# Kernel tuning notes

Measured on AMD Instinct MI355X. Metric: run time of the kernel, lower is better.

Reference implementation:

```python
import jax, jax.numpy as jnp
import numpy as np

KAPPA = 0.5


def setup_inputs() -> dict:
    key = jax.random.key(0)
    embeddings = jax.random.normal(key, (8, 4096, 64), dtype=jnp.float32)
    return {"embeddings": embeddings}


def reference(embeddings):
    # logits[b, n, m] = kappa * <emb[b,n], emb[b,m]>   -> [B, N, N]
    logits = KAPPA * jnp.einsum("bnd,bmd->bnm", embeddings, embeddings)
    B = logits.shape[0]
    # logsumexp over both matrix dims, per batch element
    loss = jax.scipy.special.logsumexp(logits.reshape(B, -1), axis=1)
    return loss.mean()
```

## Files before the change

kernel.cpp:

```cpp
#include <hip/hip_runtime.h>
#include <math.h>

#define BATCH 8
#define NTOK  4096
#define DIM   64
#define BM    128
#define NT    (NTOK / BM)
#define TPB   (NT * (NT + 1) / 2)
#define TOTAL (BATCH * TPB)
#define KAPPA 0.5f
#define LOG2E 1.4426950408889634f
#define LN2   0.6931471805599453f
#define M2FIX 48.0f

typedef _Float16 f16x8 __attribute__((ext_vector_type(8)));
typedef float    f32x16 __attribute__((ext_vector_type(16)));

__device__ __forceinline__ float EXP2(float x) {
#if __has_builtin(__builtin_amdgcn_exp2f)
    return __builtin_amdgcn_exp2f(x);
#else
    return __expf(x * LN2);
#endif
}

__global__ __launch_bounds__(256)
void conv_f16(const float* __restrict__ emb, f16x8* __restrict__ o16) {
    const size_t i = (size_t)blockIdx.x * 256 + threadIdx.x;
    const float4 v0 = *(const float4*)(emb + i * 8);
    const float4 v1 = *(const float4*)(emb + i * 8 + 4);
    f16x8 p;
    p[0] = (_Float16)v0.x; p[1] = (_Float16)v0.y;
    p[2] = (_Float16)v0.z; p[3] = (_Float16)v0.w;
    p[4] = (_Float16)v1.x; p[5] = (_Float16)v1.y;
    p[6] = (_Float16)v1.z; p[7] = (_Float16)v1.w;
    o16[i] = p;
}

__global__ __launch_bounds__(256, 4)
void gram_lse_partial(const f16x8* __restrict__ w16, float* __restrict__ ws) {
    __shared__ f16x8 S[2048];

    const int tid  = threadIdx.x;
    const int lane = tid & 63;
    const int w    = tid >> 6;
    const int p    = blockIdx.x;
    const int bb   = (p & 7) * TPB + (p >> 3);
    const int b    = bb / TPB;
    int t = bb - b * TPB;
    int ti = 0;
    while (t >= NT - ti) { t -= NT - ti; ++ti; }
    const int tj = ti + t;

    const char* pA16 = (const char*)(w16 + ((size_t)b * NTOK + (size_t)ti * BM) * 8);
    const char* pB16 = (const char*)(w16 + ((size_t)b * NTOK + (size_t)tj * BM) * 8);

    {
        const char* pbase  = (w < 2) ? pA16 : pB16;
        const int   upBase = (w & 1) * 512 + lane;
#pragma unroll
        for (int q = 0; q < 8; ++q) {
            const int up  = upBase + q * 64;
            const int g   = up >> 7;
            const int rp  = up & 127;
            const int off = (((rp ^ g) << 7) | (g << 4));
            __builtin_amdgcn_global_load_lds(
                (const __attribute__((address_space(1))) void*)(pbase + off),
                (__attribute__((address_space(3))) void*)&S[(size_t)w * 512 + q * 64],
                16, 0, 0);
        }
    }
    __syncthreads();

    const int half = lane >> 5;
    const int ln31 = lane & 31;
    const int waveR = (w & 1) * 64;
    const int waveC = (w >> 1) * 64;
    const float c2 = KAPPA * LOG2E;

    f32x16 acc00 = {}, acc01 = {}, acc10 = {}, acc11 = {};
#pragma unroll
    for (int s = 0; s < 4; ++s) {
        const int g = 2 * s + half;
        const f16x8 a0 = S[g * BM + ((waveR + ln31) ^ g)];
        const f16x8 a1 = S[g * BM + ((waveR + 32 + ln31) ^ g)];
        const f16x8 b0 = S[1024 + g * BM + ((waveC + ln31) ^ g)];
        const f16x8 b1 = S[1024 + g * BM + ((waveC + 32 + ln31) ^ g)];
        acc00 = __builtin_amdgcn_mfma_f32_32x32x16_f16(a0, b0, acc00, 0, 0, 0);
        acc01 = __builtin_amdgcn_mfma_f32_32x32x16_f16(a0, b1, acc01, 0, 0, 0);
        acc10 = __builtin_amdgcn_mfma_f32_32x32x16_f16(a1, b0, acc10, 0, 0, 0);
        acc11 = __builtin_amdgcn_mfma_f32_32x32x16_f16(a1, b1, acc11, 0, 0, 0);
    }

    float s0 = 0.f, s1 = 0.f, s2 = 0.f, s3 = 0.f;
#pragma unroll
    for (int e = 0; e < 16; ++e) {
        s0 += EXP2(fmaf(c2, acc00[e], -M2FIX));
        s1 += EXP2(fmaf(c2, acc01[e], -M2FIX));
        s2 += EXP2(fmaf(c2, acc10[e], -M2FIX));
        s3 += EXP2(fmaf(c2, acc11[e], -M2FIX));
    }
    float lsum = (s0 + s1) + (s2 + s3);
#pragma unroll
    for (int off = 32; off > 0; off >>= 1)
        lsum += __shfl_xor(lsum, off);

    if (lane == 0) {
        const float wgt = (ti == tj) ? 1.f : 2.f;
        ws[4 * (size_t)bb + w] = wgt * lsum;
    }
}

__global__ __launch_bounds__(512)
void reduce_lse(const float* __restrict__ ws, float* __restrict__ out) {
    const int tid  = threadIdx.x;
    const int w    = tid >> 6;
    const int lane = tid & 63;
    __shared__ float lse8[BATCH];

    const float* p = ws + (size_t)w * TPB * 4;
    float s = 0.f;
#pragma unroll
    for (int c = 0; c < 33; ++c) s += p[lane + 64 * c];
#pragma unroll
    for (int off = 32; off > 0; off >>= 1) s += __shfl_xor(s, off);

    if (lane == 0) lse8[w] = LN2 * (M2FIX + log2f(s));
    __syncthreads();
    if (tid == 0) {
        float a = 0.f;
        for (int i = 0; i < BATCH; ++i) a += lse8[i];
        out[0] = a * (1.f / BATCH);
    }
}

extern "C" void kernel_launch(void* const* d_in, const int* in_sizes, int n_in,
                              void* d_out, int out_size, void* d_ws, size_t ws_size,
                              hipStream_t stream) {
    const float* emb = (const float*)d_in[0];
    float* out = (float*)d_out;
    f16x8* w16 = (f16x8*)d_ws;
    float* prt = (float*)((char*)d_ws + (4u << 20));

    conv_f16<<<NTOK * BATCH * DIM / 8 / 256, 256, 0, stream>>>(emb, w16);
    gram_lse_partial<<<TOTAL, 256, 0, stream>>>(w16, prt);
    reduce_lse<<<1, 512, 0, stream>>>(prt, out);
}
```

Measured before the change: 81.11 us.

## Enlarge Gram tiles to 256x256 with 512-thread blocks

Doubles the tile edge of the symmetric Gram/logsumexp kernel from 128 to 256 rows. Blocks grow to 8 waves, and each wave now computes a 64x128 sub-tile with eight MFMA accumulators. The partial-sum layout and the final reduction are resized to match. The aim is to halve operand-staging traffic per logit and cut block count and launch overhead. In exchange, diagonal tiles waste a slightly larger share of work, each block needs 64KB of LDS, and register pressure is higher.

```diff
diff --git a/kernel.cpp b/kernel.cpp
--- a/kernel.cpp
+++ b/kernel.cpp
@@ -4,10 +4,10 @@
 #define BATCH 8
 #define NTOK  4096
 #define DIM   64
-#define BM    128
-#define NT    (NTOK / BM)
-#define TPB   (NT * (NT + 1) / 2)
-#define TOTAL (BATCH * TPB)
+#define BM    256
+#define NT2   (NTOK / BM)
+#define TPB2  (NT2 * (NT2 + 1) / 2)
+#define TOTAL2 (BATCH * TPB2)
 #define KAPPA 0.5f
 #define LOG2E 1.4426950408889634f
 #define LN2   0.6931471805599453f
@@ -37,32 +37,32 @@
     o16[i] = p;
 }
 
-__global__ __launch_bounds__(256, 4)
+__global__ __launch_bounds__(512, 2)
 void gram_lse_partial(const f16x8* __restrict__ w16, float* __restrict__ ws) {
-    __shared__ f16x8 S[2048];
+    __shared__ f16x8 S[4096];
 
     const int tid  = threadIdx.x;
     const int lane = tid & 63;
     const int w    = tid >> 6;
     const int p    = blockIdx.x;
-    const int bb   = (p & 7) * TPB + (p >> 3);
-    const int b    = bb / TPB;
-    int t = bb - b * TPB;
+    const int b    = p & 7;
+    int t = p >> 3;
     int ti = 0;
-    while (t >= NT - ti) { t -= NT - ti; ++ti; }
+    while (t >= NT2 - ti) { t -= NT2 - ti; ++ti; }
     const int tj = ti + t;
+    const int bbL = b * TPB2 + (p >> 3);
 
     const char* pA16 = (const char*)(w16 + ((size_t)b * NTOK + (size_t)ti * BM) * 8);
     const char* pB16 = (const char*)(w16 + ((size_t)b * NTOK + (size_t)tj * BM) * 8);
 
     {
-        const char* pbase  = (w < 2) ? pA16 : pB16;
-        const int   upBase = (w & 1) * 512 + lane;
+        const char* pbase  = (w < 4) ? pA16 : pB16;
+        const int   upBase = (w & 3) * 512 + lane;
 #pragma unroll
         for (int q = 0; q < 8; ++q) {
             const int up  = upBase + q * 64;
-            const int g   = up >> 7;
-            const int rp  = up & 127;
+            const int g   = up >> 8;
+            const int rp  = up & 255;
             const int off = (((rp ^ g) << 7) | (g << 4));
             __builtin_amdgcn_global_load_lds(
                 (const __attribute__((address_space(1))) void*)(pbase + off),
@@ -74,40 +74,55 @@
 
     const int half = lane >> 5;
     const int ln31 = lane & 31;
-    const int waveR = (w & 1) * 64;
-    const int waveC = (w >> 1) * 64;
+    const int wr   = w >> 1;
+    const int wc   = w & 1;
+    const int rA0  = 64 * wr + ln31, rA1 = rA0 + 32;
+    const int rB0  = 128 * wc + ln31;
     const float c2 = KAPPA * LOG2E;
 
-    f32x16 acc00 = {}, acc01 = {}, acc10 = {}, acc11 = {};
+    f32x16 acc00 = {}, acc01 = {}, acc02 = {}, acc03 = {};
+    f32x16 acc10 = {}, acc11 = {}, acc12 = {}, acc13 = {};
 #pragma unroll
     for (int s = 0; s < 4; ++s) {
         const int g = 2 * s + half;
-        const f16x8 a0 = S[g * BM + ((waveR + ln31) ^ g)];
-        const f16x8 a1 = S[g * BM + ((waveR + 32 + ln31) ^ g)];
-        const f16x8 b0 = S[1024 + g * BM + ((waveC + ln31) ^ g)];
-        const f16x8 b1 = S[1024 + g * BM + ((waveC + 32 + ln31) ^ g)];
+        const int gb = g * 256;
+        const f16x8 a0 = S[gb + (rA0 ^ g)];
+        const f16x8 a1 = S[gb + (rA1 ^ g)];
+        const f16x8 b0 = S[2048 + gb + ((rB0      ) ^ g)];
+        const f16x8 b1 = S[2048 + gb + ((rB0 + 32 ) ^ g)];
+        const f16x8 b2 = S[2048 + gb + ((rB0 + 64 ) ^ g)];
+        const f16x8 b3 = S[2048 + gb + ((rB0 + 96 ) ^ g)];
         acc00 = __builtin_amdgcn_mfma_f32_32x32x16_f16(a0, b0, acc00, 0, 0, 0);
         acc01 = __builtin_amdgcn_mfma_f32_32x32x16_f16(a0, b1, acc01, 0, 0, 0);
+        acc02 = __builtin_amdgcn_mfma_f32_32x32x16_f16(a0, b2, acc02, 0, 0, 0);
+        acc03 = __builtin_amdgcn_mfma_f32_32x32x16_f16(a0, b3, acc03, 0, 0, 0);
         acc10 = __builtin_amdgcn_mfma_f32_32x32x16_f16(a1, b0, acc10, 0, 0, 0);
         acc11 = __builtin_amdgcn_mfma_f32_32x32x16_f16(a1, b1, acc11, 0, 0, 0);
+        acc12 = __builtin_amdgcn_mfma_f32_32x32x16_f16(a1, b2, acc12, 0, 0, 0);
+        acc13 = __builtin_amdgcn_mfma_f32_32x32x16_f16(a1, b3, acc13, 0, 0, 0);
     }
 
     float s0 = 0.f, s1 = 0.f, s2 = 0.f, s3 = 0.f;
+    float s4 = 0.f, s5 = 0.f, s6 = 0.f, s7 = 0.f;
 #pragma unroll
     for (int e = 0; e < 16; ++e) {
         s0 += EXP2(fmaf(c2, acc00[e], -M2FIX));
         s1 += EXP2(fmaf(c2, acc01[e], -M2FIX));
-        s2 += EXP2(fmaf(c2, acc10[e], -M2FIX));
-        s3 += EXP2(fmaf(c2, acc11[e], -M2FIX));
+        s2 += EXP2(fmaf(c2, acc02[e], -M2FIX));
+        s3 += EXP2(fmaf(c2, acc03[e], -M2FIX));
+        s4 += EXP2(fmaf(c2, acc10[e], -M2FIX));
+        s5 += EXP2(fmaf(c2, acc11[e], -M2FIX));
+        s6 += EXP2(fmaf(c2, acc12[e], -M2FIX));
+        s7 += EXP2(fmaf(c2, acc13[e], -M2FIX));
     }
-    float lsum = (s0 + s1) + (s2 + s3);
+    float lsum = ((s0 + s1) + (s2 + s3)) + ((s4 + s5) + (s6 + s7));
 #pragma unroll
     for (int off = 32; off > 0; off >>= 1)
         lsum += __shfl_xor(lsum, off);
 
     if (lane == 0) {
         const float wgt = (ti == tj) ? 1.f : 2.f;
-        ws[4 * (size_t)bb + w] = wgt * lsum;
+        ws[8 * (size_t)bbL + w] = wgt * lsum;
     }
 }
 
@@ -118,10 +133,10 @@
     const int lane = tid & 63;
     __shared__ float lse8[BATCH];
 
-    const float* p = ws + (size_t)w * TPB * 4;
+    const float* p = ws + (size_t)w * TPB2 * 8;
     float s = 0.f;
 #pragma unroll
-    for (int c = 0; c < 33; ++c) s += p[lane + 64 * c];
+    for (int c = 0; c < 17; ++c) s += p[lane + 64 * c];
 #pragma unroll
     for (int off = 32; off > 0; off >>= 1) s += __shfl_xor(s, off);
 
@@ -143,6 +158,6 @@
     float* prt = (float*)((char*)d_ws + (4u << 20));
 
     conv_f16<<<NTOK * BATCH * DIM / 8 / 256, 256, 0, stream>>>(emb, w16);
-    gram_lse_partial<<<TOTAL, 256, 0, stream>>>(w16, prt);
+    gram_lse_partial<<<TOTAL2, 512, 0, stream>>>(w16, prt);
     reduce_lse<<<1, 512, 0, stream>>>(prt, out);
 }
```

Result: slower. 83.63 us (+3.1%).
